# Kernel tuning notes

Hardware: AMD Instinct MI355X
Metric: run time of the kernel (lower is better)

Reference implementation:

```python
import jax, jax.numpy as jnp
import numpy as np

B, S, D = 32, 512, 512
GH, LH = 8, 4            # global / local num_heads
W, STRIDE = 10, 5        # local window size and hop (window_size // 2)


def _mha(x, w_in, b_in, w_out, b_out, n_heads, key_mask=None):
    """Torch nn.MultiheadAttention (self-attn, eval mode). x: [N, L, D]."""
    N, L, d = x.shape
    dh = d // n_heads
    qkv = x @ w_in.T + b_in                       # [N, L, 3D]
    q, k, v = jnp.split(qkv, 3, axis=-1)
    def heads(t):
        return t.reshape(N, L, n_heads, dh).transpose(0, 2, 1, 3)  # [N,H,L,dh]
    q, k, v = heads(q), heads(k), heads(v)
    scores = jnp.einsum('bhqd,bhkd->bhqk', q, k) / jnp.sqrt(jnp.asarray(dh, x.dtype))
    if key_mask is not None:                      # key_mask: [N, L] bool, True = valid
        scores = jnp.where(key_mask[:, None, None, :], scores, jnp.asarray(-1e9, x.dtype))
    attn = jax.nn.softmax(scores, axis=-1)
    out = jnp.einsum('bhqk,bhkd->bhqd', attn, v).transpose(0, 2, 1, 3).reshape(N, L, d)
    return out @ w_out.T + b_out


def setup_inputs() -> dict:
    key = jax.random.key(0)
    ks = jax.random.split(key, 12)
    s = 0.02
    return {
        'x':      jax.random.normal(ks[0], (B, S, D), jnp.float32),
        'gw_in':  jax.random.normal(ks[1], (3 * D, D), jnp.float32) * s,
        'gb_in':  jnp.zeros((3 * D,), jnp.float32),
        'gw_out': jax.random.normal(ks[2], (D, D), jnp.float32) * s,
        'gb_out': jnp.zeros((D,), jnp.float32),
        'lw_in':  jax.random.normal(ks[3], (3 * D, D), jnp.float32) * s,
        'lb_in':  jnp.zeros((3 * D,), jnp.float32),
        'lw_out': jax.random.normal(ks[4], (D, D), jnp.float32) * s,
        'lb_out': jnp.zeros((D,), jnp.float32),
        'fw':     jax.random.normal(ks[5], (D, 2 * D), jnp.float32) * s,
        'fb':     jnp.zeros((D,), jnp.float32),
    }


def reference(x, gw_in, gb_in, gw_out, gb_out, lw_in, lb_in, lw_out, lb_out, fw, fb):
    # ---- global branch: full self-attention over the sequence ----
    global_out = _mha(x, gw_in, gb_in, gw_out, gb_out, GH)

    # ---- local branch: overlapping windows of size W, hop STRIDE ----
    starts = np.arange(0, S, STRIDE)              # static window starts
    NW = len(starts)
    pos = starts[:, None] + np.arange(W)          # [NW, W] absolute positions
    valid = pos < S                               # ragged tail windows
    idx = np.minimum(pos, S - 1)                  # clipped gather indices

    windows = x[:, idx]                           # [B, NW, W, D]
    windows = windows.reshape(B * NW, W, D)
    key_mask = jnp.broadcast_to(jnp.asarray(valid)[None], (B, NW, W)).reshape(B * NW, W)

    local_attn = _mha(windows, lw_in, lb_in, lw_out, lb_out, LH, key_mask=key_mask)
    local_attn = local_attn.reshape(B, NW, W, D) * jnp.asarray(valid)[None, :, :, None].astype(x.dtype)

    # scatter-add overlapping window outputs back (matches `local_out[:, i:end] +=`)
    local_out = jnp.zeros_like(x).at[:, idx.reshape(-1)].add(local_attn.reshape(B, NW * W, D))

    # ---- fusion MLP (dropout = identity in eval) ----
    combined = jnp.concatenate([global_out, local_out], axis=-1)   # [B, S, 2D]
    return jax.nn.relu(combined @ fw.T + fb)
```

## Files before the change

kernel.cpp:

```cpp
#include <hip/hip_runtime.h>
#include <cstdint>
#include <cstddef>

#define DEV __device__ __forceinline__

typedef float f32x4 __attribute__((ext_vector_type(4)));
typedef short bf16x8 __attribute__((ext_vector_type(8)));

DEV unsigned short f2bf(float f) {
  union { float f; unsigned u; } v; v.f = f;
  unsigned u = v.u;
  unsigned r = u + 0x7FFFu + ((u >> 16) & 1u);
  return (unsigned short)(r >> 16);
}
DEV float bf2f(unsigned short h) {
  union { unsigned u; float f; } v; v.u = ((unsigned)h) << 16;
  return v.f;
}
DEV unsigned cvtpk(float lo, float hi) {
  unsigned r;
  asm("v_cvt_pk_bf16_f32 %0, %1, %2" : "=v"(r) : "v"(lo), "v"(hi));
  return r;
}

DEV void gload16(const void* g, void* l) {
  __builtin_amdgcn_global_load_lds((const __attribute__((address_space(1))) unsigned int*)g,
                                   (__attribute__((address_space(3))) unsigned int*)l,
                                   16, 0, 0);
}

DEV f32x4 MFMA(bf16x8 a, bf16x8 b, f32x4 c) {
  return __builtin_amdgcn_mfma_f32_16x16x32_bf16(a, b, c, 0, 0, 0);
}

__global__ void k_f2bf(const float* __restrict__ src, unsigned short* __restrict__ dst, int n) {
  int i = (blockIdx.x * blockDim.x + threadIdx.x) * 4;
  int stride = gridDim.x * blockDim.x * 4;
  for (; i < n; i += stride) {
    float4 v = *(const float4*)(src + i);
    ushort4 o;
    o.x = f2bf(v.x); o.y = f2bf(v.y); o.z = f2bf(v.z); o.w = f2bf(v.w);
    *(ushort4*)(dst + i) = o;
  }
}

__global__ __launch_bounds__(256) void k_merge(const float* __restrict__ fw,
                                               const float* __restrict__ gw_out,
                                               const float* __restrict__ lw_out,
                                               unsigned short* __restrict__ M1b,
                                               unsigned short* __restrict__ M2b) {
  __shared__ float Fa[64][68];
  __shared__ float Gb[64][68];
  const int bi = blockIdx.x, bj = blockIdx.y, m2 = blockIdx.z;
  const float* g = m2 ? lw_out : gw_out;
  const int i0 = bi * 64, j0 = bj * 64;
  const int tid = threadIdx.x;
  const int tr = tid >> 4, tc = tid & 15;
  float acc[4][4] = {};
  for (int kc = 0; kc < 8; kc++) {
    int k0 = kc * 64;
    __syncthreads();
    #pragma unroll
    for (int it = 0; it < 4; it++) {
      int r = tr + 16 * it;
      float4 v = *(const float4*)(fw + (size_t)(i0 + r) * 1024 + m2 * 512 + k0 + tc * 4);
      Fa[tc * 4 + 0][r] = v.x; Fa[tc * 4 + 1][r] = v.y;
      Fa[tc * 4 + 2][r] = v.z; Fa[tc * 4 + 3][r] = v.w;
      *(float4*)&Gb[r][tc * 4] = *(const float4*)(g + (size_t)(k0 + r) * 512 + j0 + tc * 4);
    }
    __syncthreads();
    for (int k = 0; k < 64; k++) {
      float4 a4 = *(const float4*)&Fa[k][tr * 4];
      float4 b4 = *(const float4*)&Gb[k][tc * 4];
      float av[4] = {a4.x, a4.y, a4.z, a4.w};
      float bv[4] = {b4.x, b4.y, b4.z, b4.w};
      #pragma unroll
      for (int r = 0; r < 4; r++)
        #pragma unroll
        for (int c = 0; c < 4; c++)
          acc[r][c] += av[r] * bv[c];
    }
  }
  unsigned short* M = m2 ? M2b : M1b;
  #pragma unroll
  for (int r = 0; r < 4; r++) {
    ushort4 pk;
    pk.x = f2bf(acc[r][0]); pk.y = f2bf(acc[r][1]);
    pk.z = f2bf(acc[r][2]); pk.w = f2bf(acc[r][3]);
    *(ushort4*)&M[(size_t)(i0 + tr * 4 + r) * 512 + j0 + tc * 4] = pk;
  }
}

__global__ __launch_bounds__(256) void k_bias(const float* __restrict__ fw, const float* __restrict__ gb_out,
                                              const float* __restrict__ lb_out, const float* __restrict__ fb,
                                              float* __restrict__ bias1, float* __restrict__ bias2) {
  __shared__ float bv[512];
  const int which = blockIdx.y;
  const int i0 = blockIdx.x * 64;
  const float* src = which ? lb_out : gb_out;
  for (int t = threadIdx.x; t < 512; t += 256) bv[t] = src[t];
  __syncthreads();
  const int r = threadIdx.x >> 2, c4 = threadIdx.x & 3;
  const float* frow = fw + (size_t)(i0 + r) * 1024 + (which ? 512 : 0) + c4 * 128;
  float a = 0.f;
  #pragma unroll 4
  for (int k = 0; k < 128; k += 4) {
    float4 v = *(const float4*)(frow + k);
    a += v.x * bv[c4 * 128 + k] + v.y * bv[c4 * 128 + k + 1]
       + v.z * bv[c4 * 128 + k + 2] + v.w * bv[c4 * 128 + k + 3];
  }
  a += __shfl_xor(a, 1);
  a += __shfl_xor(a, 2);
  if (c4 == 0) {
    int i = i0 + r;
    if (which) bias2[i] = a;
    else       bias1[i] = a + fb[i];
  }
}

template <int EPI>
__global__ __launch_bounds__(256) void k_gemm(const unsigned short* __restrict__ A,
                                              const unsigned short* __restrict__ A2,
                                              const unsigned short* __restrict__ Wm,
                                              const unsigned short* __restrict__ W2,
                                              const float* __restrict__ bias,
                                              const float* __restrict__ bias2,
                                              float qscale, void* __restrict__ Cout,
                                              int Ntot, int NT) {
  __shared__ unsigned short As[2][128 * 32];
  __shared__ unsigned short Bs[2][128 * 32];
  const int tid = threadIdx.x;
  const int wave = tid >> 6, lane = tid & 63;
  const int wr = wave >> 1, wc = wave & 1;
  const int bm = blockIdx.x, bn = blockIdx.y;
  const int ql = lane & 15, kg = lane >> 4;

  const int c0 = wave * 2;
  const int srow = lane >> 2;
  const int schunk = (lane & 3) ^ ((lane >> 3) & 3);

  auto stage = [&](int buf, int t) {
    const unsigned short* sA = A;
    const unsigned short* sW = Wm;
    int k0 = t * 32;
    if (EPI == 1 && t >= 16) { sA = A2; sW = W2; k0 = (t - 16) * 32; }
    #pragma unroll
    for (int i = 0; i < 2; i++) {
      int c = c0 + i;
      int row = c * 16 + srow;
      gload16(sA + (size_t)(bm * 128 + row) * 512 + k0 + schunk * 8, &As[buf][c * 512 + lane * 8]);
      gload16(sW + (size_t)(bn * 128 + row) * 512 + k0 + schunk * 8, &Bs[buf][c * 512 + lane * 8]);
    }
  };

  const int soff = (kg ^ ((ql >> 1) & 3)) * 8;

  f32x4 acc[4][4] = {};
  stage(0, 0);
  __syncthreads();
  for (int t = 0; t < NT; t++) {
    int buf = t & 1;
    if (t + 1 < NT) stage(buf ^ 1, t + 1);
    const unsigned short* as = As[buf];
    const unsigned short* bs = Bs[buf];
    bf16x8 af[4], bfr[4];
    #pragma unroll
    for (int m = 0; m < 4; m++)
      af[m] = *(const bf16x8*)&as[(wr * 64 + m * 16 + ql) * 32 + soff];
    #pragma unroll
    for (int n = 0; n < 4; n++)
      bfr[n] = *(const bf16x8*)&bs[(wc * 64 + n * 16 + ql) * 32 + soff];
    #pragma unroll
    for (int m = 0; m < 4; m++)
      #pragma unroll
      for (int n = 0; n < 4; n++)
        acc[m][n] = MFMA(af[m], bfr[n], acc[m][n]);
    __syncthreads();
  }

  const int row0 = bm * 128 + wr * 64;
  const int col0 = bn * 128 + wc * 64;
  if (EPI == 0) {
    unsigned short* C = (unsigned short*)Cout;
    #pragma unroll
    for (int m = 0; m < 4; m++)
      #pragma unroll
      for (int n = 0; n < 4; n++) {
        int col = col0 + n * 16 + ql;
        float bcol = bias[col];
        float qs = (col < 512) ? qscale : 1.0f;
        #pragma unroll
        for (int r = 0; r < 4; r++) {
          int row = row0 + m * 16 + kg * 4 + r;
          C[(size_t)row * Ntot + col] = f2bf((acc[m][n][r] + bcol) * qs);
        }
      }
  } else {
    float* C = (float*)Cout;
    #pragma unroll
    for (int m = 0; m < 4; m++)
      #pragma unroll
      for (int n = 0; n < 4; n++) {
        int col = col0 + n * 16 + ql;
        float b1 = bias[col], b2 = bias2[col];
        #pragma unroll
        for (int r = 0; r < 4; r++) {
          int row = row0 + m * 16 + kg * 4 + r;
          float cc = ((row & 511) < 5) ? 1.0f : 2.0f;
          float v = acc[m][n][r] + b1 + cc * b2;
          C[(size_t)row * 512 + col] = fmaxf(v, 0.0f);
        }
      }
  }
}

__global__ __launch_bounds__(1024, 4) void k_attn_g(const unsigned short* __restrict__ QKV,
                                                    unsigned short* __restrict__ Og) {
  __shared__ unsigned short Klds[512 * 64];
  __shared__ unsigned short Vt[64 * 512];
  const int tid = threadIdx.x, wave = tid >> 6, lane = tid & 63;
  const int ql = lane & 15, kg = lane >> 4;
  const int h = blockIdx.x, b = blockIdx.y;
  const size_t tb = (size_t)b * 512;
  const size_t hoff = (size_t)h * 64;

  #pragma unroll
  for (int i = 0; i < 4; i++) {
    int instr = wave * 4 + i;
    int row = instr * 8 + (lane >> 3);
    int slot = lane & 7;
    int c = slot ^ (row & 7);
    gload16(QKV + (tb + row) * 1536 + 512 + hoff + c * 8, &Klds[instr * 512 + lane * 8]);
  }
  {
    int key = tid & 511;
    int cb = (tid >> 9) * 4;
    int k64 = key & 63;
    int f = k64 >> 4, kgv = (k64 >> 2) & 3, r = k64 & 3;
    int col = (key & ~63) + 32 * (f >> 1) + 4 * (f & 1) + 8 * kgv + r;
    const unsigned short* Vp = QKV + (tb + key) * 1536 + 1024 + hoff;
    #pragma unroll
    for (int c8 = 0; c8 < 4; c8++) {
      bf16x8 v8 = *(const bf16x8*)(Vp + (cb + c8) * 8);
      #pragma unroll
      for (int j = 0; j < 8; j++) {
        int d = (cb + c8) * 8 + j;
        Vt[d * 512 + (((col >> 3) ^ (d & 7)) * 8) + (col & 7)] = (unsigned short)v8[j];
      }
    }
  }
  bf16x8 qf[2][2];
  #pragma unroll
  for (int m = 0; m < 2; m++) {
    const unsigned short* Qp = QKV + (tb + wave * 32 + m * 16 + ql) * 1536 + hoff;
    qf[m][0] = *(const bf16x8*)(Qp + kg * 8);
    qf[m][1] = *(const bf16x8*)(Qp + 32 + kg * 8);
  }
  __syncthreads();

  float l_part[2] = {};
  f32x4 ot[2][4] = {};

  for (int kv = 0; kv < 8; kv++) {
    const int k0 = kv * 64;
    bf16x8 kf[4][2], vb[4][2];
    #pragma unroll
    for (int f = 0; f < 4; f++) {
      int row = k0 + 16 * f + ql;
      #pragma unroll
      for (int c = 0; c < 2; c++)
        kf[f][c] = *(const bf16x8*)&Klds[row * 64 + (((c * 4 + kg) ^ (row & 7)) * 8)];
      int d = 16 * f + ql;
      #pragma unroll
      for (int st = 0; st < 2; st++) {
        int cb_r = (k0 >> 3) + st * 4 + kg;
        vb[f][st] = *(const bf16x8*)&Vt[d * 512 + ((cb_r ^ (d & 7)) * 8)];
      }
    }
    #pragma unroll
    for (int m = 0; m < 2; m++) {
      f32x4 s[4] = {};
      #pragma unroll
      for (int f = 0; f < 4; f++) {
        s[f] = MFMA(kf[f][0], qf[m][0], s[f]);
        s[f] = MFMA(kf[f][1], qf[m][1], s[f]);
      }
      #pragma unroll
      for (int f = 0; f < 4; f++) {
        #pragma unroll
        for (int r = 0; r < 4; r++)
          s[f][r] = exp2f(s[f][r]);
        l_part[m] += (s[f][0] + s[f][1]) + (s[f][2] + s[f][3]);
      }
      #pragma unroll
      for (int st = 0; st < 2; st++) {
        union { unsigned w[4]; bf16x8 v; } pb;
        #pragma unroll
        for (int w = 0; w < 4; w++) {
          int f = 2 * st + (w >> 1);
          pb.w[w] = cvtpk(s[f][2 * (w & 1)], s[f][2 * (w & 1) + 1]);
        }
        #pragma unroll
        for (int fp = 0; fp < 4; fp++)
          ot[m][fp] = MFMA(vb[fp][st], pb.v, ot[m][fp]);
      }
    }
  }

  #pragma unroll
  for (int m = 0; m < 2; m++) {
    float l = l_part[m];
    l += __shfl_xor(l, 16);
    l += __shfl_xor(l, 32);
    float inv = 1.0f / l;
    size_t row = tb + wave * 32 + m * 16 + ql;
    #pragma unroll
    for (int fp = 0; fp < 4; fp++) {
      ushort4 st4;
      st4.x = f2bf(ot[m][fp][0] * inv);
      st4.y = f2bf(ot[m][fp][1] * inv);
      st4.z = f2bf(ot[m][fp][2] * inv);
      st4.w = f2bf(ot[m][fp][3] * inv);
      *(ushort4*)&Og[row * 512 + hoff + 16 * fp + 4 * kg] = st4;
    }
  }
}

__global__ __launch_bounds__(256) void k_attn_l(const unsigned short* __restrict__ QKV,
                                                unsigned short* __restrict__ Lacc) {
  __shared__ unsigned short Qs[5][520];
  __shared__ unsigned short Ks[15][520];
  __shared__ unsigned short Vs[15][520];
  __shared__ float Pb[2][4][5][13];
  const int w = blockIdx.x, b = blockIdx.y;
  const int p0 = 5 * w;
  const int tid = threadIdx.x;
  const size_t tbase = (size_t)b * 512;

  for (int c = tid; c < 35 * 64; c += 256) {
    int row = c >> 6, ch = (c & 63) * 8;
    if (row < 5) {
      int tok = min(p0 + row, 511);
      *(bf16x8*)&Qs[row][ch] = *(const bf16x8*)(QKV + (tbase + tok) * 1536 + ch);
    } else if (row < 20) {
      int rr = row - 5;
      int tok = min(max(p0 - 5 + rr, 0), 511);
      *(bf16x8*)&Ks[rr][ch] = *(const bf16x8*)(QKV + (tbase + tok) * 1536 + 512 + ch);
    } else {
      int rr = row - 20;
      int tok = min(max(p0 - 5 + rr, 0), 511);
      *(bf16x8*)&Vs[rr][ch] = *(const bf16x8*)(QKV + (tbase + tok) * 1536 + 1024 + ch);
    }
  }
  __syncthreads();

  #pragma unroll
  for (int rep = 0; rep < 2; rep++) {
    int idx = tid + rep * 256;
    if (idx < 400) {
      int j = idx % 10;
      int t1 = idx / 10;
      int q = t1 % 5;
      int t2 = t1 / 5;
      int h = t2 & 3;
      int win = t2 >> 2;
      int krow = win ? j : j + 5;
      int ktok = p0 - 5 + krow;
      float scv = -1e30f;
      bool ok = (win == 0 || w > 0) && (p0 + q < 512) && (ktok < 512);
      if (ok) {
        float acc = 0.f;
        const unsigned short* qp = &Qs[q][h * 128];
        const unsigned short* kp = &Ks[krow][h * 128];
        #pragma unroll
        for (int ck = 0; ck < 16; ck++) {
          bf16x8 q8 = *(const bf16x8*)(qp + ck * 8);
          bf16x8 k8 = *(const bf16x8*)(kp + ck * 8);
          #pragma unroll
          for (int e = 0; e < 8; e++)
            acc += bf2f((unsigned short)q8[e]) * bf2f((unsigned short)k8[e]);
        }
        scv = acc;
      }
      Pb[win][h][q][j] = scv;
    }
  }
  __syncthreads();

  if (tid < 40) {
    int q = tid % 5;
    int t2 = tid / 5;
    int h = t2 & 3;
    int win = t2 >> 2;
    float* row = &Pb[win][h][q][0];
    float mx = -1e30f;
    #pragma unroll
    for (int j = 0; j < 10; j++) mx = fmaxf(mx, row[j]);
    float e[10]; float su = 0.f;
    #pragma unroll
    for (int j = 0; j < 10; j++) {
      float v = row[j];
      float ej = (v <= -1e29f) ? 0.f : exp2f(v - mx);
      e[j] = ej; su += ej;
    }
    float inv = (su > 0.f) ? 1.0f / su : 0.f;
    #pragma unroll
    for (int j = 0; j < 10; j++) row[j] = e[j] * inv;
  }
  __syncthreads();

  {
    const int h = tid >> 6;
    const int d = tid * 2;
    for (int qq = 0; qq < 5; qq++) {
      int p = p0 + qq;
      if (p >= 512) break;
      float a0 = 0.f, a1 = 0.f;
      const float* P0 = &Pb[0][h][qq][0];
      #pragma unroll
      for (int j = 0; j < 10; j++) {
        float pw = P0[j];
        a0 += pw * bf2f(Vs[j + 5][d]);
        a1 += pw * bf2f(Vs[j + 5][d + 1]);
      }
      if (w > 0) {
        const float* P1 = &Pb[1][h][qq][0];
        #pragma unroll
        for (int j = 0; j < 10; j++) {
          float pw = P1[j];
          a0 += pw * bf2f(Vs[j][d]);
          a1 += pw * bf2f(Vs[j][d + 1]);
        }
      }
      ushort2 st; st.x = f2bf(a0); st.y = f2bf(a1);
      *(ushort2*)&Lacc[(tbase + p) * 512 + d] = st;
    }
  }
}

extern "C" void kernel_launch(void* const* d_in, const int* in_sizes, int n_in,
                              void* d_out, int out_size, void* d_ws, size_t ws_size,
                              hipStream_t stream) {
  const float* x      = (const float*)d_in[0];
  const float* gw_in  = (const float*)d_in[1];
  const float* gb_in  = (const float*)d_in[2];
  const float* gw_out = (const float*)d_in[3];
  const float* gb_out = (const float*)d_in[4];
  const float* lw_in  = (const float*)d_in[5];
  const float* lb_in  = (const float*)d_in[6];
  const float* lw_out = (const float*)d_in[7];
  const float* lb_out = (const float*)d_in[8];
  const float* fw     = (const float*)d_in[9];
  const float* fb     = (const float*)d_in[10];

  char* ws = (char*)d_ws;
  auto alloc = [&](size_t bytes) -> char* {
    char* p = ws;
    ws += (bytes + 255) & ~(size_t)255;
    return p;
  };
  unsigned short* xb     = (unsigned short*)alloc((size_t)16384 * 512 * 2);
  unsigned short* gwin_b = (unsigned short*)alloc((size_t)1536 * 512 * 2);
  unsigned short* lwin_b = (unsigned short*)alloc((size_t)1536 * 512 * 2);
  unsigned short* M1b    = (unsigned short*)alloc((size_t)512 * 512 * 2);
  unsigned short* M2b    = (unsigned short*)alloc((size_t)512 * 512 * 2);
  float* bias1           = (float*)alloc(512 * 4);
  float* bias2           = (float*)alloc(512 * 4);
  unsigned short* QKV    = (unsigned short*)alloc((size_t)16384 * 1536 * 2);
  unsigned short* Og     = (unsigned short*)alloc((size_t)16384 * 512 * 2);
  unsigned short* La     = (unsigned short*)alloc((size_t)16384 * 512 * 2);

  k_f2bf<<<2048, 256, 0, stream>>>(x, xb, 16384 * 512);
  k_f2bf<<<128, 256, 0, stream>>>(gw_in, gwin_b, 1536 * 512);
  k_f2bf<<<128, 256, 0, stream>>>(lw_in, lwin_b, 1536 * 512);
  k_merge<<<dim3(8, 8, 2), 256, 0, stream>>>(fw, gw_out, lw_out, M1b, M2b);
  k_bias<<<dim3(8, 2), 256, 0, stream>>>(fw, gb_out, lb_out, fb, bias1, bias2);

  k_gemm<0><<<dim3(128, 12), 256, 0, stream>>>(xb, nullptr, gwin_b, nullptr, gb_in, nullptr,
                                               0.125f * 1.44269504f, QKV, 1536, 16);
  k_attn_g<<<dim3(8, 32), 1024, 0, stream>>>(QKV, Og);

  k_gemm<0><<<dim3(128, 12), 256, 0, stream>>>(xb, nullptr, lwin_b, nullptr, lb_in, nullptr,
                                               0.08838834764831845f * 1.44269504f, QKV, 1536, 16);
  k_attn_l<<<dim3(103, 32), 256, 0, stream>>>(QKV, La);

  k_gemm<1><<<dim3(128, 4), 256, 0, stream>>>(Og, La, M1b, M2b, bias1, bias2,
                                              1.0f, d_out, 512, 32);
}
```

Before: 214.1 us.

## Use 8 waves per GEMM block and vectorize epilogue via transposed MFMA

The GEMM kernel moves from 4 waves to 8 waves per 128x128 tile, so each wave now owns a 64x32 sub-tile and a single 16-byte global-to-LDS load per thread per stage. MFMA operands are swapped so that each lane holds 4 consecutive columns, which lets the epilogue write bias-added outputs as ushort4/float4 vector stores instead of scalar strided stores. The aim is more latency hiding per CU and fewer store instructions. In exchange, the waves read more redundant A fragments from LDS and each block uses more threads.

After: 223.8 us. 1.05x slower.

```diff
diff --git a/kernel.cpp b/kernel.cpp
--- a/kernel.cpp
+++ b/kernel.cpp
@@ -119,7 +119,7 @@
 }
 
 template <int EPI>
-__global__ __launch_bounds__(256) void k_gemm(const unsigned short* __restrict__ A,
+__global__ __launch_bounds__(512) void k_gemm(const unsigned short* __restrict__ A,
                                               const unsigned short* __restrict__ A2,
                                               const unsigned short* __restrict__ Wm,
                                               const unsigned short* __restrict__ W2,
@@ -131,31 +131,25 @@
   __shared__ unsigned short Bs[2][128 * 32];
   const int tid = threadIdx.x;
   const int wave = tid >> 6, lane = tid & 63;
-  const int wr = wave >> 1, wc = wave & 1;
+  const int wr = wave >> 2, wc = wave & 3;
   const int bm = blockIdx.x, bn = blockIdx.y;
   const int ql = lane & 15, kg = lane >> 4;
 
-  const int c0 = wave * 2;
-  const int srow = lane >> 2;
-  const int schunk = (lane & 3) ^ ((lane >> 3) & 3);
+  const int srow = tid >> 2;
+  const int schunk = (tid & 3) ^ ((srow >> 1) & 3);
 
   auto stage = [&](int buf, int t) {
     const unsigned short* sA = A;
     const unsigned short* sW = Wm;
     int k0 = t * 32;
     if (EPI == 1 && t >= 16) { sA = A2; sW = W2; k0 = (t - 16) * 32; }
-    #pragma unroll
-    for (int i = 0; i < 2; i++) {
-      int c = c0 + i;
-      int row = c * 16 + srow;
-      gload16(sA + (size_t)(bm * 128 + row) * 512 + k0 + schunk * 8, &As[buf][c * 512 + lane * 8]);
-      gload16(sW + (size_t)(bn * 128 + row) * 512 + k0 + schunk * 8, &Bs[buf][c * 512 + lane * 8]);
-    }
+    gload16(sA + (size_t)(bm * 128 + srow) * 512 + k0 + schunk * 8, &As[buf][tid * 8]);
+    gload16(sW + (size_t)(bn * 128 + srow) * 512 + k0 + schunk * 8, &Bs[buf][tid * 8]);
   };
 
   const int soff = (kg ^ ((ql >> 1) & 3)) * 8;
 
-  f32x4 acc[4][4] = {};
+  f32x4 acc[4][2] = {};
   stage(0, 0);
   __syncthreads();
   for (int t = 0; t < NT; t++) {
@@ -163,54 +157,60 @@
     if (t + 1 < NT) stage(buf ^ 1, t + 1);
     const unsigned short* as = As[buf];
     const unsigned short* bs = Bs[buf];
-    bf16x8 af[4], bfr[4];
+    bf16x8 af[4], bfr[2];
     #pragma unroll
     for (int m = 0; m < 4; m++)
       af[m] = *(const bf16x8*)&as[(wr * 64 + m * 16 + ql) * 32 + soff];
     #pragma unroll
-    for (int n = 0; n < 4; n++)
-      bfr[n] = *(const bf16x8*)&bs[(wc * 64 + n * 16 + ql) * 32 + soff];
+    for (int n = 0; n < 2; n++)
+      bfr[n] = *(const bf16x8*)&bs[(wc * 32 + n * 16 + ql) * 32 + soff];
     #pragma unroll
     for (int m = 0; m < 4; m++)
       #pragma unroll
-      for (int n = 0; n < 4; n++)
-        acc[m][n] = MFMA(af[m], bfr[n], acc[m][n]);
+      for (int n = 0; n < 2; n++)
+        acc[m][n] = MFMA(bfr[n], af[m], acc[m][n]);
     __syncthreads();
   }
 
   const int row0 = bm * 128 + wr * 64;
-  const int col0 = bn * 128 + wc * 64;
+  const int colb = bn * 128 + wc * 32;
   if (EPI == 0) {
     unsigned short* C = (unsigned short*)Cout;
     #pragma unroll
-    for (int m = 0; m < 4; m++)
-      #pragma unroll
-      for (int n = 0; n < 4; n++) {
-        int col = col0 + n * 16 + ql;
-        float bcol = bias[col];
-        float qs = (col < 512) ? qscale : 1.0f;
-        #pragma unroll
-        for (int r = 0; r < 4; r++) {
-          int row = row0 + m * 16 + kg * 4 + r;
-          C[(size_t)row * Ntot + col] = f2bf((acc[m][n][r] + bcol) * qs);
-        }
-      }
+    for (int mq = 0; mq < 4; mq++) {
+      int row = row0 + mq * 16 + ql;
+      #pragma unroll
+      for (int nq = 0; nq < 2; nq++) {
+        int cg = colb + nq * 16 + kg * 4;
+        float4 b4 = *(const float4*)&bias[cg];
+        float qs = (cg < 512) ? qscale : 1.0f;
+        ushort4 o;
+        o.x = f2bf((acc[mq][nq][0] + b4.x) * qs);
+        o.y = f2bf((acc[mq][nq][1] + b4.y) * qs);
+        o.z = f2bf((acc[mq][nq][2] + b4.z) * qs);
+        o.w = f2bf((acc[mq][nq][3] + b4.w) * qs);
+        *(ushort4*)&C[(size_t)row * Ntot + cg] = o;
+      }
+    }
   } else {
     float* C = (float*)Cout;
     #pragma unroll
-    for (int m = 0; m < 4; m++)
-      #pragma unroll
-      for (int n = 0; n < 4; n++) {
-        int col = col0 + n * 16 + ql;
-        float b1 = bias[col], b2 = bias2[col];
-        #pragma unroll
-        for (int r = 0; r < 4; r++) {
-          int row = row0 + m * 16 + kg * 4 + r;
-          float cc = ((row & 511) < 5) ? 1.0f : 2.0f;
-          float v = acc[m][n][r] + b1 + cc * b2;
-          C[(size_t)row * 512 + col] = fmaxf(v, 0.0f);
-        }
-      }
+    for (int mq = 0; mq < 4; mq++) {
+      int row = row0 + mq * 16 + ql;
+      float cc = ((row & 511) < 5) ? 1.0f : 2.0f;
+      #pragma unroll
+      for (int nq = 0; nq < 2; nq++) {
+        int cg = colb + nq * 16 + kg * 4;
+        float4 b1 = *(const float4*)&bias[cg];
+        float4 b2 = *(const float4*)&bias2[cg];
+        float4 v;
+        v.x = fmaxf(acc[mq][nq][0] + b1.x + cc * b2.x, 0.0f);
+        v.y = fmaxf(acc[mq][nq][1] + b1.y + cc * b2.y, 0.0f);
+        v.z = fmaxf(acc[mq][nq][2] + b1.z + cc * b2.z, 0.0f);
+        v.w = fmaxf(acc[mq][nq][3] + b1.w + cc * b2.w, 0.0f);
+        *(float4*)&C[(size_t)row * 512 + cg] = v;
+      }
+    }
   }
 }
 
@@ -476,14 +476,14 @@
   k_merge<<<dim3(8, 8, 2), 256, 0, stream>>>(fw, gw_out, lw_out, M1b, M2b);
   k_bias<<<dim3(8, 2), 256, 0, stream>>>(fw, gb_out, lb_out, fb, bias1, bias2);
 
-  k_gemm<0><<<dim3(128, 12), 256, 0, stream>>>(xb, nullptr, gwin_b, nullptr, gb_in, nullptr,
+  k_gemm<0><<<dim3(128, 12), 512, 0, stream>>>(xb, nullptr, gwin_b, nullptr, gb_in, nullptr,
                                                0.125f * 1.44269504f, QKV, 1536, 16);
   k_attn_g<<<dim3(8, 32), 1024, 0, stream>>>(QKV, Og);
 
-  k_gemm<0><<<dim3(128, 12), 256, 0, stream>>>(xb, nullptr, lwin_b, nullptr, lb_in, nullptr,
+  k_gemm<0><<<dim3(128, 12), 512, 0, stream>>>(xb, nullptr, lwin_b, nullptr, lb_in, nullptr,
                                                0.08838834764831845f * 1.44269504f, QKV, 1536, 16);
   k_attn_l<<<dim3(103, 32), 256, 0, stream>>>(QKV, La);
 
-  k_gemm<1><<<dim3(128, 4), 256, 0, stream>>>(Og, La, M1b, M2b, bias1, bias2,
+  k_gemm<1><<<dim3(128, 4), 512, 0, stream>>>(Og, La, M1b, M2b, bias1, bias2,
                                               1.0f, d_out, 512, 32);
 }
```
